# Optimization experiments

Measured on AMD Instinct MI355X. Metric: run time of the kernel, lower is better.

The kernel has to match this reference:

```python
import jax, jax.numpy as jnp
import numpy as np

B, N, D, H, NB = 64, 2048, 256, 64, 3
TOPK_RATIO = 0.1
LN_EPS = 1e-5
NEG_INF = -1e30


def setup_inputs() -> dict:
    key = jax.random.key(0)
    ks = jax.random.split(key, 16)
    s = 0.02
    return {
        "instances": jax.random.normal(ks[0], (B, N, D), dtype=jnp.float32),
        "mask": jnp.ones((B, N), dtype=jnp.float32),
        # top-k scorer: Linear(D,64) -> ReLU -> Linear(64,1)
        "Ws1": jax.random.normal(ks[1], (D, H), dtype=jnp.float32) * s,
        "bs1": jnp.zeros((H,), dtype=jnp.float32),
        "Ws2": jax.random.normal(ks[2], (H,), dtype=jnp.float32) * s,
        "bs2": jnp.zeros((), dtype=jnp.float32),
        # NB attention branches stacked: Linear(D,64) -> Tanh -> Linear(64,1)
        "Wa1": jax.random.normal(ks[3], (NB, D, H), dtype=jnp.float32) * s,
        "ba1": jnp.zeros((NB, H), dtype=jnp.float32),
        "Wa2": jax.random.normal(ks[4], (NB, H), dtype=jnp.float32) * s,
        "ba2": jnp.zeros((NB,), dtype=jnp.float32),
        # fusion: Linear(5D, 2D) -> LayerNorm -> GELU -> Linear(2D, 2D)
        "Wf1": jax.random.normal(ks[5], ((2 + NB) * D, 2 * D), dtype=jnp.float32) * s,
        "bf1": jnp.zeros((2 * D,), dtype=jnp.float32),
        "ln_g": jnp.ones((2 * D,), dtype=jnp.float32),
        "ln_b": jnp.zeros((2 * D,), dtype=jnp.float32),
        "Wf2": jax.random.normal(ks[6], (2 * D, 2 * D), dtype=jnp.float32) * s,
        "bf2": jnp.zeros((2 * D,), dtype=jnp.float32),
    }


def _forward(instances, mask, Ws1, bs1, Ws2, bs2, Wa1, ba1, Wa2, ba2,
             Wf1, bf1, ln_g, ln_b, Wf2, bf2):
    invalid = mask == 0  # [B, N]

    # ---- mean pooling (masked) ----
    valid_counts = jnp.sum(mask, axis=1, keepdims=True)  # [B,1]
    mean_pooled = jnp.einsum("bnd,bn->bd", instances, mask) / jnp.maximum(valid_counts, 1.0)

    # ---- top-k pooling ----
    h = jax.nn.relu(jnp.einsum("bnd,dh->bnh", instances, Ws1) + bs1)
    tk_scores = jnp.einsum("bnh,h->bn", h, Ws2) + bs2  # [B, N]
    tk_scores = jnp.where(invalid, NEG_INF, tk_scores)
    # torch code computes per-sample k but only uses max_k; with all-ones mask
    # max_k == int(N * ratio) (static) -- replicated faithfully.
    max_k = max(1, int(N * TOPK_RATIO))
    _, topk_idx = jax.lax.top_k(tk_scores, max_k)  # [B, max_k]
    topk_mask = jnp.zeros((B, N), dtype=instances.dtype)
    topk_mask = topk_mask.at[jnp.arange(B)[:, None], topk_idx].set(1.0)
    combined = topk_mask * mask
    denom = jnp.maximum(jnp.sum(combined, axis=1, keepdims=True), 1.0)
    topk_pooled = jnp.einsum("bnd,bn->bd", instances, combined) / denom

    # ---- multi-branch attention (vectorized over branches) ----
    ah = jnp.tanh(jnp.einsum("bnd,kdh->kbnh", instances, Wa1) + ba1[:, None, None, :])
    a_scores = jnp.einsum("kbnh,kh->kbn", ah, Wa2) + ba2[:, None, None]  # [NB,B,N]
    a_scores = jnp.where(invalid[None], NEG_INF, a_scores)
    attn = jax.nn.softmax(a_scores, axis=-1)
    attn = jnp.where(invalid[None], 0.0, attn)  # [NB, B, N]
    branch_pooled = jnp.einsum("kbn,bnd->kbd", attn, instances)  # [NB, B, D]

    # ---- fusion MLP ----
    cat = jnp.concatenate(
        [mean_pooled, topk_pooled, branch_pooled.transpose(1, 0, 2).reshape(B, NB * D)],
        axis=-1,
    )  # [B, (2+NB)*D]
    x = cat @ Wf1 + bf1
    mu = jnp.mean(x, axis=-1, keepdims=True)
    var = jnp.mean(jnp.square(x - mu), axis=-1, keepdims=True)
    x = (x - mu) * jax.lax.rsqrt(var + LN_EPS) * ln_g + ln_b
    x = jax.nn.gelu(x, approximate=False)  # torch nn.GELU default = exact erf
    bag_embedding = x @ Wf2 + bf2  # [B, 2D]

    # ---- attention diagnostics ----
    all_attn = attn.transpose(1, 0, 2)  # [B, NB, N]
    avg_attn = jnp.mean(all_attn, axis=1)  # [B, N]
    entropy = -jnp.sum(avg_attn * jnp.log(avg_attn + 1e-8), axis=-1)
    effective_n = 1.0 / jnp.sum(jnp.square(avg_attn), axis=-1)
    k5 = max(1, int(N * 0.05))
    top5_mass = jnp.sum(jax.lax.top_k(avg_attn, k5)[0], axis=-1)
    return bag_embedding, all_attn, avg_attn, topk_mask, entropy, effective_n, top5_mass


def reference(instances, mask, Ws1, bs1, Ws2, bs2, Wa1, ba1, Wa2, ba2,
              Wf1, bf1, ln_g, ln_b, Wf2, bf2):
    return _forward(instances, mask, Ws1, bs1, Ws2, bs2, Wa1, ba1, Wa2, ba2,
                    Wf1, bf1, ln_g, ln_b, Wf2, bf2)
```

## Files before the change

### kernel.cpp

```cpp
#include <hip/hip_runtime.h>
#include <stdint.h>

constexpr int B_ = 64, N_ = 2048, D_ = 256, H_ = 64;
constexpr int M_ = B_ * N_;
constexpr int TOPK_ = 204, TOP5_ = 102;
constexpr float NEGINF_ = -1e30f;

constexpr int OUT_BAG  = 0;
constexpr int OUT_ATTN = 32768;
constexpr int OUT_AVG  = OUT_ATTN + 393216;
constexpr int OUT_TOPK = OUT_AVG + 131072;
constexpr int OUT_ENT  = OUT_TOPK + 131072;
constexpr int OUT_EFF  = OUT_ENT + 64;
constexpr int OUT_T5   = OUT_EFF + 64;

constexpr int WS_TK    = 0;
constexpr int WS_SC    = 131072;
constexpr int WS_STATS = WS_SC + 393216;
constexpr int WS_PART  = WS_STATS + 128;
constexpr int WS_BFRAG = WS_PART + 655360;
constexpr int WS_X1    = WS_BFRAG + 32768;
constexpr int WS_G     = WS_X1 + 32768;

typedef short  bf16x8 __attribute__((ext_vector_type(8)));
typedef float  f32x4  __attribute__((ext_vector_type(4)));

__device__ __forceinline__ short cvt_bf16(float f) {
    unsigned u = __float_as_uint(f);
    unsigned r = (u + 0x7FFFu + ((u >> 16) & 1u)) >> 16;
    return (short)r;
}
__device__ __forceinline__ float tanh_fast(float x) {
    float e = __expf(2.0f * x);
    return 1.0f - 2.0f / (e + 1.0f);
}
__device__ __forceinline__ unsigned flip_f32(float f) {
    unsigned u = __float_as_uint(f);
    return (u & 0x80000000u) ? ~u : (u | 0x80000000u);
}
__device__ __forceinline__ float unflip_f32(unsigned u) {
    unsigned b = (u & 0x80000000u) ? (u & 0x7FFFFFFFu) : ~u;
    return __uint_as_float(b);
}

__device__ __forceinline__ float block_sum256(float v, volatile float* red, int t) {
    #pragma unroll
    for (int off = 32; off; off >>= 1) v += __shfl_xor(v, off, 64);
    __syncthreads();
    if ((t & 63) == 0) red[t >> 6] = v;
    __syncthreads();
    return red[0] + red[1] + red[2] + red[3];
}
__device__ __forceinline__ float block_max256(float v, volatile float* red, int t) {
    #pragma unroll
    for (int off = 32; off; off >>= 1) v = fmaxf(v, __shfl_xor(v, off, 64));
    __syncthreads();
    if ((t & 63) == 0) red[t >> 6] = v;
    __syncthreads();
    return fmaxf(fmaxf(red[0], red[1]), fmaxf(red[2], red[3]));
}

__device__ unsigned radix_kth(const unsigned* key, int n, int k,
                              unsigned* hist, int* sdig, int t, int* rem_out)
{
    unsigned prefix = 0;
    int kk = k;
    #pragma unroll
    for (int pass = 0; pass < 4; ++pass) {
        const int shift = 24 - 8 * pass;
        const unsigned hi_mask = (pass == 0) ? 0u : (0xFFFFFFFFu << (shift + 8));
        hist[t] = 0;
        __syncthreads();
        for (int i = t; i < n; i += 256) {
            unsigned u = key[i];
            if ((u & hi_mask) == (prefix & hi_mask))
                atomicAdd(&hist[(u >> shift) & 0xFFu], 1u);
        }
        __syncthreads();
        for (int s = 1; s < 256; s <<= 1) {
            unsigned v = (t + s < 256) ? hist[t + s] : 0u;
            __syncthreads();
            hist[t] += v;
            __syncthreads();
        }
        if (t == 0) *sdig = 0;
        __syncthreads();
        if ((int)hist[t] >= kk) atomicMax(sdig, t);
        __syncthreads();
        const int dig = *sdig;
        if (dig < 255) kk -= (int)hist[dig + 1];
        prefix |= (unsigned)dig << shift;
        __syncthreads();
    }
    *rem_out = kk;
    return prefix;
}

__global__ __launch_bounds__(256)
void k_prep(const float* __restrict__ Ws1, const float* __restrict__ Wa1,
            short* __restrict__ wsB)
{
    const int id = blockIdx.x * 256 + threadIdx.x;
    if (id >= 16384) return;
    const int lane = id & 63, ct = (id >> 6) & 15, c = id >> 10;
    const int col = ct * 16 + (lane & 15);
    const int kb  = c * 32 + ((lane >> 4) << 3);
    bf16x8 v;
    #pragma unroll
    for (int j = 0; j < 8; ++j) {
        const int k = kb + j;
        float w = (col < 64) ? Ws1[(size_t)k * H_ + col]
                             : Wa1[(((size_t)(col >> 6) - 1) * D_ + k) * H_ + (col & 63)];
        v[j] = cvt_bf16(w);
    }
    *(bf16x8*)(wsB + (size_t)id * 8) = v;
}

__global__ __launch_bounds__(256, 4)
void k_scores(const float* __restrict__ inst, const float* __restrict__ mask,
              const short* __restrict__ wsB,
              const float* __restrict__ bs1, const float* __restrict__ Ws2,
              const float* __restrict__ bs2,
              const float* __restrict__ ba1, const float* __restrict__ Wa2,
              const float* __restrict__ ba2,
              float* __restrict__ ws)
{
    __shared__ short lbs[16 * 64 * 8];
    const int t = threadIdx.x;
    const int w = t >> 6, l = t & 63;
    const int rg = l >> 4, li = l & 15;
    const int row0 = blockIdx.x * 64;
    const int myrow = row0 + w * 16 + li;

    f32x4 acc[16];
    #pragma unroll
    for (int ct = 0; ct < 16; ++ct) acc[ct] = (f32x4){0.f, 0.f, 0.f, 0.f};

    const float* xrow = inst + (size_t)myrow * D_;

    for (int c = 0; c < 8; ++c) {
        {
            float4* dst = (float4*)lbs;
            const float4* src = (const float4*)(wsB + (size_t)c * 8192);
            #pragma unroll
            for (int i = 0; i < 4; ++i) dst[t + 256 * i] = src[t + 256 * i];
        }
        __syncthreads();

        const int kb = c * 32 + rg * 8;
        float4 x0 = *(const float4*)(xrow + kb);
        float4 x1 = *(const float4*)(xrow + kb + 4);
        bf16x8 a;
        a[0] = cvt_bf16(x0.x); a[1] = cvt_bf16(x0.y);
        a[2] = cvt_bf16(x0.z); a[3] = cvt_bf16(x0.w);
        a[4] = cvt_bf16(x1.x); a[5] = cvt_bf16(x1.y);
        a[6] = cvt_bf16(x1.z); a[7] = cvt_bf16(x1.w);

        #pragma unroll
        for (int ct = 0; ct < 16; ++ct) {
            bf16x8 b = ((const bf16x8*)lbs)[ct * 64 + l];
            acc[ct] = __builtin_amdgcn_mfma_f32_16x16x32_bf16(a, b, acc[ct], 0, 0, 0);
        }
        __syncthreads();
    }

    float bias[16], w2v[16];
    #pragma unroll
    for (int ct = 0; ct < 16; ++ct) {
        const int col = ct * 16 + li;
        const int s = col >> 6, h = col & 63;
        if (s == 0) { bias[ct] = bs1[h];               w2v[ct] = Ws2[h]; }
        else        { bias[ct] = ba1[(s - 1) * H_ + h]; w2v[ct] = Wa2[(s - 1) * H_ + h]; }
    }
    const float bs2_v = bs2[0];
    float ba2_v[3] = {ba2[0], ba2[1], ba2[2]};

    #pragma unroll
    for (int s = 0; s < 4; ++s) {
        float res[4];
        #pragma unroll
        for (int i = 0; i < 4; ++i) {
            float p = 0.0f;
            #pragma unroll
            for (int q = 0; q < 4; ++q) {
                const int ct = s * 4 + q;
                float v = acc[ct][i] + bias[ct];
                p += (s == 0 ? fmaxf(v, 0.0f) : tanh_fast(v)) * w2v[ct];
            }
            #pragma unroll
            for (int off = 1; off < 16; off <<= 1) p += __shfl_xor(p, off, 64);
            res[i] = p;
        }
        if (li == 0) {
            #pragma unroll
            for (int i = 0; i < 4; ++i) {
                const int gr = row0 + w * 16 + rg * 4 + i;
                const bool inv = (mask[gr] == 0.0f);
                float val = res[i] + (s == 0 ? bs2_v : ba2_v[s - 1]);
                float* dst = (s == 0) ? (ws + WS_TK + gr)
                                      : (ws + WS_SC + (size_t)(s - 1) * M_ + gr);
                *dst = inv ? NEGINF_ : val;
            }
        }
    }
}

__global__ __launch_bounds__(256)
void k_topk(const float* __restrict__ ws_tk, const float* __restrict__ mask,
            float* __restrict__ out_topk, float* __restrict__ ws_stats)
{
    __shared__ unsigned ukey[N_];
    __shared__ unsigned hist[256];
    __shared__ int sdig;
    __shared__ int tie_cnt;
    __shared__ float red[4];
    const int b = blockIdx.x, t = threadIdx.x;
    float vsum = 0.0f;
    for (int i = t; i < N_; i += 256) {
        ukey[i] = flip_f32(ws_tk[b * N_ + i]);
        vsum += mask[b * N_ + i];
        out_topk[b * N_ + i] = 0.0f;
    }
    float vs = block_sum256(vsum, red, t);
    if (t == 0) { ws_stats[b] = vs; tie_cnt = 0; }
    __syncthreads();
    int rem;
    const unsigned T = radix_kth(ukey, N_, TOPK_, hist, &sdig, t, &rem);
    float csum = 0.0f;
    for (int i = t; i < N_; i += 256) {
        const unsigned u = ukey[i];
        bool take = (u > T);
        if (!take && u == T) take = (atomicAdd(&tie_cnt, 1) < rem);
        if (take) {
            out_topk[b * N_ + i] = 1.0f;
            csum += mask[b * N_ + i];
        }
    }
    float cs = block_sum256(csum, red, t);
    if (t == 0) ws_stats[64 + b] = cs;
}

__global__ __launch_bounds__(256)
void k_softmax(const float* __restrict__ ws_sc, float* __restrict__ out_attn)
{
    __shared__ float red[4];
    const int sb = blockIdx.x;
    const int s = sb >> 6, b = sb & 63;
    const int t = threadIdx.x;
    const float* src = ws_sc + (size_t)sb * N_;
    float fv[8];
    float mx = -3.4e38f;
    #pragma unroll
    for (int m = 0; m < 8; ++m) { fv[m] = src[t + 256 * m]; mx = fmaxf(mx, fv[m]); }
    float bm = block_max256(mx, red, t);
    float sm = 0.0f;
    #pragma unroll
    for (int m = 0; m < 8; ++m) { fv[m] = expf(fv[m] - bm); sm += fv[m]; }
    float tot = block_sum256(sm, red, t);
    float inv = 1.0f / tot;
    float* dst = out_attn + ((size_t)b * 3 + s) * N_;
    #pragma unroll
    for (int m = 0; m < 8; ++m) dst[t + 256 * m] = fv[m] * inv;
}

__global__ __launch_bounds__(256)
void k_pool(const float* __restrict__ inst, const float* __restrict__ mask,
            const float* __restrict__ out_topk, const float* __restrict__ out_attn,
            float* __restrict__ ws_part)
{
    __shared__ float wgt[5][256];
    __shared__ float4 partial[4][5][64];
    const int blk = blockIdx.x;
    const int b = blk >> 3, ch = blk & 7;
    const int n0 = ch * 256;
    const int t = threadIdx.x;
    const int w = t >> 6, l = t & 63;
    {
        float mv = mask[b * N_ + n0 + t];
        wgt[0][t] = mv;
        wgt[1][t] = out_topk[b * N_ + n0 + t] * mv;
        const float* ab = out_attn + (size_t)b * 3 * N_ + n0 + t;
        wgt[2][t] = ab[0];
        wgt[3][t] = ab[N_];
        wgt[4][t] = ab[2 * N_];
    }
    __syncthreads();
    float4 a0 = {0,0,0,0}, a1 = {0,0,0,0}, a2 = {0,0,0,0}, a3 = {0,0,0,0}, a4 = {0,0,0,0};
    const float4* xp = (const float4*)(inst + ((size_t)b * N_ + n0 + w * 64) * D_) + l;
    #pragma unroll 4
    for (int nn = 0; nn < 64; ++nn) {
        float4 x = xp[(size_t)nn * 64];
        float w0 = wgt[0][w * 64 + nn], w1 = wgt[1][w * 64 + nn];
        float w2 = wgt[2][w * 64 + nn], w3 = wgt[3][w * 64 + nn];
        float w4 = wgt[4][w * 64 + nn];
        a0.x = fmaf(x.x, w0, a0.x); a0.y = fmaf(x.y, w0, a0.y);
        a0.z = fmaf(x.z, w0, a0.z); a0.w = fmaf(x.w, w0, a0.w);
        a1.x = fmaf(x.x, w1, a1.x); a1.y = fmaf(x.y, w1, a1.y);
        a1.z = fmaf(x.z, w1, a1.z); a1.w = fmaf(x.w, w1, a1.w);
        a2.x = fmaf(x.x, w2, a2.x); a2.y = fmaf(x.y, w2, a2.y);
        a2.z = fmaf(x.z, w2, a2.z); a2.w = fmaf(x.w, w2, a2.w);
        a3.x = fmaf(x.x, w3, a3.x); a3.y = fmaf(x.y, w3, a3.y);
        a3.z = fmaf(x.z, w3, a3.z); a3.w = fmaf(x.w, w3, a3.w);
        a4.x = fmaf(x.x, w4, a4.x); a4.y = fmaf(x.y, w4, a4.y);
        a4.z = fmaf(x.z, w4, a4.z); a4.w = fmaf(x.w, w4, a4.w);
    }
    partial[w][0][l] = a0; partial[w][1][l] = a1; partial[w][2][l] = a2;
    partial[w][3][l] = a3; partial[w][4][l] = a4;
    __syncthreads();
    for (int idx = t; idx < 320; idx += 256) {
        const int j = idx >> 6, l2 = idx & 63;
        float4 s0 = partial[0][j][l2], s1 = partial[1][j][l2];
        float4 s2 = partial[2][j][l2], s3 = partial[3][j][l2];
        float4 sm;
        sm.x = s0.x + s1.x + s2.x + s3.x;
        sm.y = s0.y + s1.y + s2.y + s3.y;
        sm.z = s0.z + s1.z + s2.z + s3.z;
        sm.w = s0.w + s1.w + s2.w + s3.w;
        *(float4*)(ws_part + (size_t)blk * 1280 + j * 256 + l2 * 4) = sm;
    }
}

__global__ __launch_bounds__(256)
void k_diag(const float* __restrict__ out_attn, float* __restrict__ out_avg,
            float* __restrict__ out_ent, float* __restrict__ out_eff,
            float* __restrict__ out_t5)
{
    __shared__ unsigned ukey[N_];
    __shared__ unsigned hist[256];
    __shared__ int sdig;
    __shared__ float red[4];
    const int b = blockIdx.x, t = threadIdx.x;
    const float* a0 = out_attn + (size_t)b * 3 * N_;
    float esum = 0.0f, qsum = 0.0f;
    for (int i = t; i < N_; i += 256) {
        float a = (a0[i] + a0[N_ + i] + a0[2 * N_ + i]) * (1.0f / 3.0f);
        out_avg[b * N_ + i] = a;
        esum -= a * logf(a + 1e-8f);
        qsum += a * a;
        ukey[i] = flip_f32(a);
    }
    float es = block_sum256(esum, red, t);
    float qs = block_sum256(qsum, red, t);
    if (t == 0) { out_ent[b] = es; out_eff[b] = 1.0f / qs; }
    __syncthreads();
    int rem;
    const unsigned T = radix_kth(ukey, N_, TOP5_, hist, &sdig, t, &rem);
    float tsum = 0.0f;
    for (int i = t; i < N_; i += 256) {
        const unsigned u = ukey[i];
        if (u > T) tsum += unflip_f32(u);
    }
    float ts = block_sum256(tsum, red, t);
    if (t == 0) out_t5[b] = ts + (float)rem * unflip_f32(T);
}

__global__ __launch_bounds__(256)
void k_fuse1(const float* __restrict__ ws_part, const float* __restrict__ ws_stats,
             const float* __restrict__ Wf1, const float* __restrict__ bf1,
             float* __restrict__ x1)
{
    __shared__ float cl[1280];
    __shared__ float part[256];
    const int blk = blockIdx.x;
    const int b = blk >> 3, c = blk & 7;
    const int t = threadIdx.x;
    const float inv0 = 1.0f / fmaxf(ws_stats[b], 1.0f);
    const float inv1 = 1.0f / fmaxf(ws_stats[64 + b], 1.0f);
    for (int i = t; i < 1280; i += 256) {
        const int j = i >> 8, d = i & 255;
        float s = 0.0f;
        #pragma unroll
        for (int cc = 0; cc < 8; ++cc)
            s += ws_part[((size_t)(b * 8 + cc) * 5 + j) * 256 + d];
        if (j == 0)      s *= inv0;
        else if (j == 1) s *= inv1;
        cl[i] = s;
    }
    __syncthreads();
    const int j = c * 64 + (t & 63);
    const int s = t >> 6;
    float acc = 0.0f;
    const float* wp = Wf1 + (size_t)(s * 320) * 512 + j;
    #pragma unroll 8
    for (int i = 0; i < 320; ++i)
        acc = fmaf(cl[s * 320 + i], wp[(size_t)i * 512], acc);
    part[t] = acc;
    __syncthreads();
    if (t < 64)
        x1[b * 512 + c * 64 + t] =
            part[t] + part[64 + t] + part[128 + t] + part[192 + t] + bf1[c * 64 + t];
}

__global__ __launch_bounds__(256)
void k_fuse2(const float* __restrict__ x1, const float* __restrict__ ln_g,
             const float* __restrict__ ln_b, float* __restrict__ g)
{
    __shared__ float red[4];
    const int b = blockIdx.x, t = threadIdx.x;
    float v0 = x1[b * 512 + t], v1 = x1[b * 512 + 256 + t];
    float mu = block_sum256(v0 + v1, red, t) * (1.0f / 512.0f);
    float d0 = v0 - mu, d1 = v1 - mu;
    float var = block_sum256(d0 * d0 + d1 * d1, red, t) * (1.0f / 512.0f);
    float is = 1.0f / sqrtf(var + 1e-5f);
    float y0 = d0 * is * ln_g[t] + ln_b[t];
    float y1 = d1 * is * ln_g[t + 256] + ln_b[t + 256];
    g[b * 512 + t]       = 0.5f * y0 * (1.0f + erff(y0 * 0.70710678118654752440f));
    g[b * 512 + 256 + t] = 0.5f * y1 * (1.0f + erff(y1 * 0.70710678118654752440f));
}

__global__ __launch_bounds__(256)
void k_fuse3(const float* __restrict__ g, const float* __restrict__ Wf2,
             const float* __restrict__ bf2, float* __restrict__ out_bag)
{
    __shared__ float gl[512];
    __shared__ float part[256];
    const int blk = blockIdx.x;
    const int b = blk >> 3, c = blk & 7;
    const int t = threadIdx.x;
    const int j = c * 64 + (t & 63);
    const int s = t >> 6;
    for (int i = t; i < 512; i += 256) gl[i] = g[b * 512 + i];
    __syncthreads();
    float acc = 0.0f;
    const float* wp = Wf2 + (size_t)(s * 128) * 512 + j;
    #pragma unroll 8
    for (int i = 0; i < 128; ++i)
        acc = fmaf(gl[s * 128 + i], wp[(size_t)i * 512], acc);
    part[t] = acc;
    __syncthreads();
    if (t < 64)
        out_bag[b * 512 + c * 64 + t] =
            part[t] + part[64 + t] + part[128 + t] + part[192 + t] + bf2[c * 64 + t];
}

extern "C" void kernel_launch(void* const* d_in, const int* in_sizes, int n_in,
                              void* d_out, int out_size, void* d_ws, size_t ws_size,
                              hipStream_t stream)
{
    (void)in_sizes; (void)n_in; (void)out_size; (void)ws_size;
    const float* inst = (const float*)d_in[0];
    const float* mask = (const float*)d_in[1];
    const float* Ws1  = (const float*)d_in[2];
    const float* bs1  = (const float*)d_in[3];
    const float* Ws2  = (const float*)d_in[4];
    const float* bs2  = (const float*)d_in[5];
    const float* Wa1  = (const float*)d_in[6];
    const float* ba1  = (const float*)d_in[7];
    const float* Wa2  = (const float*)d_in[8];
    const float* ba2  = (const float*)d_in[9];
    const float* Wf1  = (const float*)d_in[10];
    const float* bf1  = (const float*)d_in[11];
    const float* lng  = (const float*)d_in[12];
    const float* lnb  = (const float*)d_in[13];
    const float* Wf2  = (const float*)d_in[14];
    const float* bf2  = (const float*)d_in[15];

    float* out = (float*)d_out;
    float* ws  = (float*)d_ws;
    short* wsB = (short*)(ws + WS_BFRAG);

    k_prep<<<64, 256, 0, stream>>>(Ws1, Wa1, wsB);
    k_scores<<<M_ / 64, 256, 0, stream>>>(inst, mask, wsB, bs1, Ws2, bs2,
                                          ba1, Wa2, ba2, ws);
    k_topk<<<B_, 256, 0, stream>>>(ws + WS_TK, mask, out + OUT_TOPK, ws + WS_STATS);
    k_softmax<<<3 * B_, 256, 0, stream>>>(ws + WS_SC, out + OUT_ATTN);
    k_pool<<<B_ * 8, 256, 0, stream>>>(inst, mask, out + OUT_TOPK, out + OUT_ATTN,
                                       ws + WS_PART);
    k_diag<<<B_, 256, 0, stream>>>(out + OUT_ATTN, out + OUT_AVG, out + OUT_ENT,
                                   out + OUT_EFF, out + OUT_T5);
    k_fuse1<<<B_ * 8, 256, 0, stream>>>(ws + WS_PART, ws + WS_STATS, Wf1, bf1,
                                        ws + WS_X1);
    k_fuse2<<<B_, 256, 0, stream>>>(ws + WS_X1, lng, lnb, ws + WS_G);
    k_fuse3<<<B_ * 8, 256, 0, stream>>>(ws + WS_G, Wf2, bf2, out + OUT_BAG);
}
```

Measured before the change: 343.1 us.

## Restructure score GEMM with LDS-staged activations and fuse topk/softmax/diag kernels

The score kernel now stages a 64-row tile of activations into LDS as bf16 once. Each wave takes one 64-column head slice, holds its weight fragments in registers read straight from global memory, and prefetches the next K-chunk. This replaces the per-chunk LDS weight copies and barriers, and the epilogue now reduces one head per wave. Separately, the top-k, softmax and diagnostics kernels are merged into one per-batch kernel that keeps the attention rows in shared memory, removing two launches and the re-read of attention from global memory. The cost is that softmax now runs on 64 blocks instead of 192, which lowers parallelism for that stage, and the score kernel needs more registers and LDS.

```diff
diff --git a/kernel.cpp b/kernel.cpp
--- a/kernel.cpp
+++ b/kernel.cpp
@@ -29,6 +29,9 @@
     unsigned u = __float_as_uint(f);
     unsigned r = (u + 0x7FFFu + ((u >> 16) & 1u)) >> 16;
     return (short)r;
+}
+__device__ __forceinline__ unsigned pack_bf16x2(float a, float b) {
+    return (unsigned)(unsigned short)cvt_bf16(a) | ((unsigned)(unsigned short)cvt_bf16(b) << 16);
 }
 __device__ __forceinline__ float tanh_fast(float x) {
     float e = __expf(2.0f * x);
@@ -116,7 +119,7 @@
     *(bf16x8*)(wsB + (size_t)id * 8) = v;
 }
 
-__global__ __launch_bounds__(256, 4)
+__global__ __launch_bounds__(256)
 void k_scores(const float* __restrict__ inst, const float* __restrict__ mask,
               const short* __restrict__ wsB,
               const float* __restrict__ bs1, const float* __restrict__ Ws2,
@@ -125,96 +128,100 @@
               const float* __restrict__ ba2,
               float* __restrict__ ws)
 {
-    __shared__ short lbs[16 * 64 * 8];
+    __shared__ unsigned xas[8192];
     const int t = threadIdx.x;
-    const int w = t >> 6, l = t & 63;
-    const int rg = l >> 4, li = l & 15;
+    const int s = t >> 6, l = t & 63;
+    const int li = l & 15, qu = l >> 4;
     const int row0 = blockIdx.x * 64;
-    const int myrow = row0 + w * 16 + li;
-
-    f32x4 acc[16];
-    #pragma unroll
-    for (int ct = 0; ct < 16; ++ct) acc[ct] = (f32x4){0.f, 0.f, 0.f, 0.f};
-
-    const float* xrow = inst + (size_t)myrow * D_;
-
+
+    {
+        const float4* src = (const float4*)(inst + (size_t)row0 * D_);
+        #pragma unroll
+        for (int i = 0; i < 16; ++i) {
+            const int f = i * 256 + t;
+            const int row = f >> 6, k4 = f & 63;
+            float4 x = src[f];
+            const int base = ((k4 >> 3) * 256) + ((row >> 4) * 64) + (((k4 >> 1) & 3) * 16) + (row & 15);
+            const int ui = base * 4 + (k4 & 1) * 2;
+            xas[ui]     = pack_bf16x2(x.x, x.y);
+            xas[ui + 1] = pack_bf16x2(x.z, x.w);
+        }
+    }
+    __syncthreads();
+
+    f32x4 acc[4][4];
+    #pragma unroll
+    for (int rt = 0; rt < 4; ++rt)
+        #pragma unroll
+        for (int c4 = 0; c4 < 4; ++c4) acc[rt][c4] = (f32x4){0.f, 0.f, 0.f, 0.f};
+
+    const bf16x8* Bg = (const bf16x8*)wsB;
+    bf16x8 bcur[4], bnxt[4];
+    #pragma unroll
+    for (int c4 = 0; c4 < 4; ++c4) bcur[c4] = Bg[(0 * 16 + s * 4 + c4) * 64 + l];
+
+    #pragma unroll
     for (int c = 0; c < 8; ++c) {
-        {
-            float4* dst = (float4*)lbs;
-            const float4* src = (const float4*)(wsB + (size_t)c * 8192);
+        if (c < 7) {
             #pragma unroll
-            for (int i = 0; i < 4; ++i) dst[t + 256 * i] = src[t + 256 * i];
-        }
-        __syncthreads();
-
-        const int kb = c * 32 + rg * 8;
-        float4 x0 = *(const float4*)(xrow + kb);
-        float4 x1 = *(const float4*)(xrow + kb + 4);
-        bf16x8 a;
-        a[0] = cvt_bf16(x0.x); a[1] = cvt_bf16(x0.y);
-        a[2] = cvt_bf16(x0.z); a[3] = cvt_bf16(x0.w);
-        a[4] = cvt_bf16(x1.x); a[5] = cvt_bf16(x1.y);
-        a[6] = cvt_bf16(x1.z); a[7] = cvt_bf16(x1.w);
-
-        #pragma unroll
-        for (int ct = 0; ct < 16; ++ct) {
-            bf16x8 b = ((const bf16x8*)lbs)[ct * 64 + l];
-            acc[ct] = __builtin_amdgcn_mfma_f32_16x16x32_bf16(a, b, acc[ct], 0, 0, 0);
-        }
-        __syncthreads();
-    }
-
-    float bias[16], w2v[16];
-    #pragma unroll
-    for (int ct = 0; ct < 16; ++ct) {
-        const int col = ct * 16 + li;
-        const int s = col >> 6, h = col & 63;
-        if (s == 0) { bias[ct] = bs1[h];               w2v[ct] = Ws2[h]; }
-        else        { bias[ct] = ba1[(s - 1) * H_ + h]; w2v[ct] = Wa2[(s - 1) * H_ + h]; }
-    }
-    const float bs2_v = bs2[0];
-    float ba2_v[3] = {ba2[0], ba2[1], ba2[2]};
-
-    #pragma unroll
-    for (int s = 0; s < 4; ++s) {
-        float res[4];
+            for (int c4 = 0; c4 < 4; ++c4) bnxt[c4] = Bg[((c + 1) * 16 + s * 4 + c4) * 64 + l];
+        }
+        #pragma unroll
+        for (int rt = 0; rt < 4; ++rt) {
+            bf16x8 a = ((const bf16x8*)xas)[(c * 4 + rt) * 64 + l];
+            #pragma unroll
+            for (int c4 = 0; c4 < 4; ++c4)
+                acc[rt][c4] = __builtin_amdgcn_mfma_f32_16x16x32_bf16(a, bcur[c4], acc[rt][c4], 0, 0, 0);
+        }
+        #pragma unroll
+        for (int c4 = 0; c4 < 4; ++c4) bcur[c4] = bnxt[c4];
+    }
+
+    float bias[4], w2v[4];
+    #pragma unroll
+    for (int c4 = 0; c4 < 4; ++c4) {
+        const int h = c4 * 16 + li;
+        if (s == 0) { bias[c4] = bs1[h];                w2v[c4] = Ws2[h]; }
+        else        { bias[c4] = ba1[(s - 1) * H_ + h]; w2v[c4] = Wa2[(s - 1) * H_ + h]; }
+    }
+    const float b2 = (s == 0) ? bs2[0] : ba2[s - 1];
+    float* dst = (s == 0) ? (ws + WS_TK) : (ws + WS_SC + (size_t)(s - 1) * M_);
+
+    #pragma unroll
+    for (int rt = 0; rt < 4; ++rt) {
         #pragma unroll
         for (int i = 0; i < 4; ++i) {
             float p = 0.0f;
             #pragma unroll
-            for (int q = 0; q < 4; ++q) {
-                const int ct = s * 4 + q;
-                float v = acc[ct][i] + bias[ct];
-                p += (s == 0 ? fmaxf(v, 0.0f) : tanh_fast(v)) * w2v[ct];
+            for (int c4 = 0; c4 < 4; ++c4) {
+                float v = acc[rt][c4][i] + bias[c4];
+                p += (s == 0 ? fmaxf(v, 0.0f) : tanh_fast(v)) * w2v[c4];
             }
             #pragma unroll
             for (int off = 1; off < 16; off <<= 1) p += __shfl_xor(p, off, 64);
-            res[i] = p;
-        }
-        if (li == 0) {
-            #pragma unroll
-            for (int i = 0; i < 4; ++i) {
-                const int gr = row0 + w * 16 + rg * 4 + i;
-                const bool inv = (mask[gr] == 0.0f);
-                float val = res[i] + (s == 0 ? bs2_v : ba2_v[s - 1]);
-                float* dst = (s == 0) ? (ws + WS_TK + gr)
-                                      : (ws + WS_SC + (size_t)(s - 1) * M_ + gr);
-                *dst = inv ? NEGINF_ : val;
+            if (li == 0) {
+                const int gr = row0 + rt * 16 + qu * 4 + i;
+                dst[gr] = (mask[gr] == 0.0f) ? NEGINF_ : (p + b2);
             }
         }
     }
 }
 
 __global__ __launch_bounds__(256)
-void k_topk(const float* __restrict__ ws_tk, const float* __restrict__ mask,
-            float* __restrict__ out_topk, float* __restrict__ ws_stats)
-{
+void k_batch(const float* __restrict__ ws_tk, const float* __restrict__ ws_sc,
+             const float* __restrict__ mask,
+             float* __restrict__ out_topk, float* __restrict__ ws_stats,
+             float* __restrict__ out_attn, float* __restrict__ out_avg,
+             float* __restrict__ out_ent, float* __restrict__ out_eff,
+             float* __restrict__ out_t5)
+{
+    __shared__ float attn_s[3][N_];
     __shared__ unsigned ukey[N_];
     __shared__ unsigned hist[256];
-    __shared__ int sdig;
-    __shared__ int tie_cnt;
+    __shared__ int sdig, tie_cnt;
     __shared__ float red[4];
     const int b = blockIdx.x, t = threadIdx.x;
+
     float vsum = 0.0f;
     for (int i = t; i < N_; i += 256) {
         ukey[i] = flip_f32(ws_tk[b * N_ + i]);
@@ -225,7 +232,7 @@
     if (t == 0) { ws_stats[b] = vs; tie_cnt = 0; }
     __syncthreads();
     int rem;
-    const unsigned T = radix_kth(ukey, N_, TOPK_, hist, &sdig, t, &rem);
+    unsigned T = radix_kth(ukey, N_, TOPK_, hist, &sdig, t, &rem);
     float csum = 0.0f;
     for (int i = t; i < N_; i += 256) {
         const unsigned u = ukey[i];
@@ -238,29 +245,49 @@
     }
     float cs = block_sum256(csum, red, t);
     if (t == 0) ws_stats[64 + b] = cs;
-}
-
-__global__ __launch_bounds__(256)
-void k_softmax(const float* __restrict__ ws_sc, float* __restrict__ out_attn)
-{
-    __shared__ float red[4];
-    const int sb = blockIdx.x;
-    const int s = sb >> 6, b = sb & 63;
-    const int t = threadIdx.x;
-    const float* src = ws_sc + (size_t)sb * N_;
-    float fv[8];
-    float mx = -3.4e38f;
-    #pragma unroll
-    for (int m = 0; m < 8; ++m) { fv[m] = src[t + 256 * m]; mx = fmaxf(mx, fv[m]); }
-    float bm = block_max256(mx, red, t);
-    float sm = 0.0f;
-    #pragma unroll
-    for (int m = 0; m < 8; ++m) { fv[m] = expf(fv[m] - bm); sm += fv[m]; }
-    float tot = block_sum256(sm, red, t);
-    float inv = 1.0f / tot;
-    float* dst = out_attn + ((size_t)b * 3 + s) * N_;
-    #pragma unroll
-    for (int m = 0; m < 8; ++m) dst[t + 256 * m] = fv[m] * inv;
+
+    for (int s = 0; s < 3; ++s) {
+        const float* src = ws_sc + ((size_t)s * B_ + b) * N_;
+        float fv[8];
+        float mx = -3.4e38f;
+        #pragma unroll
+        for (int m = 0; m < 8; ++m) { fv[m] = src[t + 256 * m]; mx = fmaxf(mx, fv[m]); }
+        float bm = block_max256(mx, red, t);
+        float sm = 0.0f;
+        #pragma unroll
+        for (int m = 0; m < 8; ++m) { fv[m] = expf(fv[m] - bm); sm += fv[m]; }
+        float tot = block_sum256(sm, red, t);
+        float inv = 1.0f / tot;
+        float* dst = out_attn + ((size_t)b * 3 + s) * N_;
+        #pragma unroll
+        for (int m = 0; m < 8; ++m) {
+            float a = fv[m] * inv;
+            attn_s[s][t + 256 * m] = a;
+            dst[t + 256 * m] = a;
+        }
+    }
+    __syncthreads();
+
+    float esum = 0.0f, qsum = 0.0f;
+    for (int i = t; i < N_; i += 256) {
+        float a = (attn_s[0][i] + attn_s[1][i] + attn_s[2][i]) * (1.0f / 3.0f);
+        out_avg[b * N_ + i] = a;
+        esum -= a * logf(a + 1e-8f);
+        qsum += a * a;
+        ukey[i] = flip_f32(a);
+    }
+    float es = block_sum256(esum, red, t);
+    float qs = block_sum256(qsum, red, t);
+    if (t == 0) { out_ent[b] = es; out_eff[b] = 1.0f / qs; }
+    __syncthreads();
+    T = radix_kth(ukey, N_, TOP5_, hist, &sdig, t, &rem);
+    float tsum = 0.0f;
+    for (int i = t; i < N_; i += 256) {
+        const unsigned u = ukey[i];
+        if (u > T) tsum += unflip_f32(u);
+    }
+    float ts = block_sum256(tsum, red, t);
+    if (t == 0) out_t5[b] = ts + (float)rem * unflip_f32(T);
 }
 
 __global__ __launch_bounds__(256)
@@ -321,40 +348,6 @@
 }
 
 __global__ __launch_bounds__(256)
-void k_diag(const float* __restrict__ out_attn, float* __restrict__ out_avg,
-            float* __restrict__ out_ent, float* __restrict__ out_eff,
-            float* __restrict__ out_t5)
-{
-    __shared__ unsigned ukey[N_];
-    __shared__ unsigned hist[256];
-    __shared__ int sdig;
-    __shared__ float red[4];
-    const int b = blockIdx.x, t = threadIdx.x;
-    const float* a0 = out_attn + (size_t)b * 3 * N_;
-    float esum = 0.0f, qsum = 0.0f;
-    for (int i = t; i < N_; i += 256) {
-        float a = (a0[i] + a0[N_ + i] + a0[2 * N_ + i]) * (1.0f / 3.0f);
-        out_avg[b * N_ + i] = a;
-        esum -= a * logf(a + 1e-8f);
-        qsum += a * a;
-        ukey[i] = flip_f32(a);
-    }
-    float es = block_sum256(esum, red, t);
-    float qs = block_sum256(qsum, red, t);
-    if (t == 0) { out_ent[b] = es; out_eff[b] = 1.0f / qs; }
-    __syncthreads();
-    int rem;
-    const unsigned T = radix_kth(ukey, N_, TOP5_, hist, &sdig, t, &rem);
-    float tsum = 0.0f;
-    for (int i = t; i < N_; i += 256) {
-        const unsigned u = ukey[i];
-        if (u > T) tsum += unflip_f32(u);
-    }
-    float ts = block_sum256(tsum, red, t);
-    if (t == 0) out_t5[b] = ts + (float)rem * unflip_f32(T);
-}
-
-__global__ __launch_bounds__(256)
 void k_fuse1(const float* __restrict__ ws_part, const float* __restrict__ ws_stats,
              const float* __restrict__ Wf1, const float* __restrict__ bf1,
              float* __restrict__ x1)
@@ -462,12 +455,12 @@
     k_prep<<<64, 256, 0, stream>>>(Ws1, Wa1, wsB);
     k_scores<<<M_ / 64, 256, 0, stream>>>(inst, mask, wsB, bs1, Ws2, bs2,
                                           ba1, Wa2, ba2, ws);
-    k_topk<<<B_, 256, 0, stream>>>(ws + WS_TK, mask, out + OUT_TOPK, ws + WS_STATS);
-    k_softmax<<<3 * B_, 256, 0, stream>>>(ws + WS_SC, out + OUT_ATTN);
+    k_batch<<<B_, 256, 0, stream>>>(ws + WS_TK, ws + WS_SC, mask,
+                                    out + OUT_TOPK, ws + WS_STATS,
+                                    out + OUT_ATTN, out + OUT_AVG,
+                                    out + OUT_ENT, out + OUT_EFF, out + OUT_T5);
     k_pool<<<B_ * 8, 256, 0, stream>>>(inst, mask, out + OUT_TOPK, out + OUT_ATTN,
                                        ws + WS_PART);
-    k_diag<<<B_, 256, 0, stream>>>(out + OUT_ATTN, out + OUT_AVG, out + OUT_ENT,
-                                   out + OUT_EFF, out + OUT_T5);
     k_fuse1<<<B_ * 8, 256, 0, stream>>>(ws + WS_PART, ws + WS_STATS, Wf1, bf1,
                                         ws + WS_X1);
     k_fuse2<<<B_, 256, 0, stream>>>(ws + WS_X1, lng, lnb, ws + WS_G);
```

After: 347.4 us. No clear change (+1.2%).
